# Kernel tuning notes

Hardware: AMD Instinct MI355X
Metric: run time of the kernel (lower is better)

The kernel has to match this reference:

```python
import jax, jax.numpy as jnp
import numpy as np

FA, FB_CAT, FM, HID = 133, 147, 8, 100  # atom feat, bond feat (concat), mol feat, hidden
N_ATOMS, N_BONDS, N_MOLS, MAX_NB = 250000, 500000, 10000, 6
DEPTH = 3


def setup_inputs() -> dict:
    key = jax.random.key(0)
    ks = jax.random.split(key, 10)
    f_atoms = jax.random.normal(ks[0], (N_ATOMS, FA), jnp.float32)
    f_bonds = jax.random.normal(ks[1], (N_BONDS, FB_CAT), jnp.float32)
    f_mol = jax.random.normal(ks[2], (N_MOLS, FM), jnp.float32)
    a2b = jax.random.randint(ks[3], (N_ATOMS, MAX_NB), 0, N_BONDS, jnp.int32)
    b2a = jax.random.randint(ks[4], (N_BONDS,), 0, N_ATOMS, jnp.int32)
    b2revb = jax.random.randint(ks[5], (N_BONDS,), 0, N_BONDS, jnp.int32)
    # contiguous molecules of 25 atoms each -> equivalent of ascope segments
    mol_id = (jnp.arange(N_ATOMS, dtype=jnp.int32) // (N_ATOMS // N_MOLS))
    # parameters (Linear with bias=False): stored as (in, out)
    W_i = jax.random.normal(ks[6], (FB_CAT, HID), jnp.float32) * 0.05
    W_h = jax.random.normal(ks[7], (HID, HID), jnp.float32) * 0.05
    W_o = jax.random.normal(ks[8], (HID + FA, HID), jnp.float32) * 0.05
    return {"f_atoms": f_atoms, "f_bonds": f_bonds, "f_mol": f_mol,
            "W_i": W_i, "W_h": W_h, "W_o": W_o,
            "a2b": a2b, "b2a": b2a, "b2revb": b2revb,
            "mol_id": mol_id, "n_mols": N_MOLS}


def reference(f_atoms, f_bonds, f_mol, W_i, W_h, W_o, a2b, b2a, b2revb, mol_id, n_mols):
    act = jax.nn.relu
    inp = act(f_bonds @ W_i)              # (B, H)
    message = inp
    for _ in range(DEPTH - 1):
        nei = message[a2b]                # (A, MAX_NB, H) gather
        a_message = nei.sum(axis=1)       # (A, H)
        message = a_message[b2a] - message[b2revb]  # (B, H)
        message = act(inp + message @ W_h)
        # dropout p=0 (eval) -> identity
    # readout to atoms
    a_message = message[a2b].sum(axis=1)  # (A, H)
    a_input = jnp.concatenate([f_atoms, a_message], axis=1)  # (A, FA+H)
    atom_hiddens = act(a_input @ W_o)     # (A, H)
    # per-molecule mean over ragged segments (ascope equivalent)
    mol_sum = jax.ops.segment_sum(atom_hiddens, mol_id, num_segments=n_mols)
    counts = jax.ops.segment_sum(jnp.ones((atom_hiddens.shape[0],), atom_hiddens.dtype),
                                 mol_id, num_segments=n_mols)
    mol_vecs = mol_sum / jnp.maximum(counts, 1.0)[:, None]  # zero-vec for empty mols
    mol_vecs = jnp.concatenate([mol_vecs, f_mol], axis=1)   # (M, H+FM)
    return mol_vecs, atom_hiddens
```

## Files before the change

### kernel.cpp

```cpp
#include <hip/hip_runtime.h>

#define THREADS 256

typedef __bf16 bf16x8 __attribute__((ext_vector_type(8)));
typedef float f32x4 __attribute__((ext_vector_type(4)));
typedef float f32x4u __attribute__((ext_vector_type(4), aligned(4)));

__device__ __forceinline__ unsigned short f2b(float x) {
    unsigned int u = __float_as_uint(x);
    u = (u + 0x7FFFu + ((u >> 16) & 1u)) >> 16;
    return (unsigned short)u;
}
__device__ __forceinline__ float b2f(unsigned short h) {
    return __uint_as_float(((unsigned int)h) << 16);
}
__device__ __forceinline__ bf16x8 as_bf(uint4 q) {
    union { uint4 q; bf16x8 v; } u; u.q = q; return u.v;
}

__global__ __launch_bounds__(64) void pack_w(const float* __restrict__ W,
                                             unsigned short* __restrict__ out, int K)
{
    int bid = blockIdx.x;
    int kc = bid / 7, nt = bid - kc * 7;
    int l = threadIdx.x;
    int k0 = kc * 32 + (l >> 4) * 8;
    int n = nt * 16 + (l & 15);
    unsigned short v[8];
    #pragma unroll
    for (int j = 0; j < 8; ++j) {
        int k = k0 + j;
        float x = (k < K && n < 100) ? W[(size_t)k * 100 + n] : 0.f;
        v[j] = f2b(x);
    }
    *(uint4*)&out[((size_t)bid * 64 + l) * 8] = *(uint4*)v;
}

__global__ __launch_bounds__(64) void pack_wo(const float* __restrict__ W,
                                              unsigned short* __restrict__ out)
{
    int bid = blockIdx.x;
    int kc = bid / 7, nt = bid - kc * 7;
    int l = threadIdx.x;
    int k0 = kc * 32 + (l >> 4) * 8;
    int n = nt * 16 + (l & 15);
    unsigned short v[8];
    #pragma unroll
    for (int j = 0; j < 8; ++j) {
        int k = k0 + j;
        float x = 0.f;
        if (n < 100) {
            if (k < 100)                 x = W[(size_t)(133 + k) * 100 + n];
            else if (k >= 112 && k < 245) x = W[(size_t)(k - 112) * 100 + n];
        }
        v[j] = f2b(x);
    }
    *(uint4*)&out[((size_t)bid * 64 + l) * 8] = *(uint4*)v;
}

__global__ __launch_bounds__(THREADS) void gather_sum_bf16(
    const unsigned short* __restrict__ msg, const int* __restrict__ a2b,
    unsigned short* __restrict__ amsg, int A)
{
    int t = blockIdx.x * THREADS + threadIdx.x;
    if (t >= A * 14) return;
    int a = t / 14;
    int c = t - a * 14;
    const int* nb = a2b + (size_t)a * 6;
    float s[8];
    #pragma unroll
    for (int e = 0; e < 8; ++e) s[e] = 0.f;
    #pragma unroll
    for (int j = 0; j < 6; ++j) {
        uint4 v = *(const uint4*)&msg[(size_t)nb[j] * 112 + c * 8];
        const unsigned short* pv = (const unsigned short*)&v;
        #pragma unroll
        for (int e = 0; e < 8; ++e) s[e] += b2f(pv[e]);
    }
    unsigned short r[8];
    #pragma unroll
    for (int e = 0; e < 8; ++e) r[e] = f2b(s[e]);
    *(uint4*)&amsg[(size_t)a * 112 + c * 8] = *(uint4*)r;
}

__global__ __launch_bounds__(THREADS) void gemm_in(
    const float* __restrict__ fb, const unsigned short* __restrict__ wf,
    unsigned short* __restrict__ Y, int M)
{
    __shared__ unsigned short Os[64 * 136];
    const int tid = threadIdx.x;
    const int l = tid & 63, w = tid >> 6;
    const int quad = l >> 4, c15 = l & 15;
    const int row0 = blockIdx.x * 64;
    const int rc = min(row0 + w * 16 + c15, M - 1);
    const float* rowp = fb + (size_t)rc * 147;

    uint4 af[5];
    #pragma unroll
    for (int kc = 0; kc < 4; ++kc) {
        f32x4u x0 = *(const f32x4u*)(rowp + kc * 32 + quad * 8);
        f32x4u x1 = *(const f32x4u*)(rowp + kc * 32 + quad * 8 + 4);
        unsigned short t[8];
        #pragma unroll
        for (int e = 0; e < 4; ++e) { t[e] = f2b(x0[e]); t[4 + e] = f2b(x1[e]); }
        af[kc] = *(uint4*)t;
    }
    {
        unsigned short t[8];
        #pragma unroll
        for (int j = 0; j < 8; ++j) {
            int k = 128 + quad * 8 + j;
            t[j] = (k < 147) ? f2b(rowp[k]) : (unsigned short)0;
        }
        af[4] = *(uint4*)t;
    }

    f32x4 acc[7];
    #pragma unroll
    for (int nt = 0; nt < 7; ++nt) acc[nt] = (f32x4){0.f, 0.f, 0.f, 0.f};
    #pragma unroll
    for (int kc = 0; kc < 5; ++kc) {
        #pragma unroll
        for (int nt = 0; nt < 7; ++nt) {
            uint4 bq = *(const uint4*)&wf[((size_t)(kc * 7 + nt) * 64 + l) * 8];
            acc[nt] = __builtin_amdgcn_mfma_f32_16x16x32_bf16(as_bf(af[kc]), as_bf(bq), acc[nt], 0, 0, 0);
        }
    }

    #pragma unroll
    for (int nt = 0; nt < 7; ++nt)
        #pragma unroll
        for (int reg = 0; reg < 4; ++reg)
            Os[(w * 16 + quad * 4 + reg) * 136 + nt * 16 + c15] = f2b(fmaxf(acc[nt][reg], 0.f));
    __syncthreads();

    for (int t = tid; t < 64 * 14; t += THREADS) {
        int rl = t / 14, c = t - rl * 14;
        int rr = row0 + rl;
        if (rr < M)
            *(uint4*)&Y[(size_t)rr * 112 + c * 8] = *(const uint4*)&Os[rl * 136 + c * 8];
    }
}

__global__ __launch_bounds__(THREADS) void gemm_msg(
    const unsigned short* __restrict__ amsg, const unsigned short* __restrict__ msg,
    const int* __restrict__ b2a, const int* __restrict__ b2revb,
    const unsigned short* __restrict__ wf, const unsigned short* __restrict__ bias,
    unsigned short* __restrict__ Y, int M)
{
    __shared__ unsigned short Os[64 * 136];
    const int tid = threadIdx.x;
    const int l = tid & 63, w = tid >> 6;
    const int quad = l >> 4, c15 = l & 15;
    const int row0 = blockIdx.x * 64;
    const int rc = min(row0 + w * 16 + c15, M - 1);
    const int iA = b2a[rc], iB = b2revb[rc];
    const unsigned short* pa = amsg + (size_t)iA * 112 + quad * 8;
    const unsigned short* pb = msg  + (size_t)iB * 112 + quad * 8;

    uint4 a1[4], a2[4];
    #pragma unroll
    for (int kc = 0; kc < 4; ++kc) {
        a1[kc] = *(const uint4*)(pa + kc * 32);
        a2[kc] = *(const uint4*)(pb + kc * 32);
    }

    f32x4 acc1[7], acc2[7];
    #pragma unroll
    for (int nt = 0; nt < 7; ++nt) {
        acc1[nt] = (f32x4){0.f, 0.f, 0.f, 0.f};
        acc2[nt] = (f32x4){0.f, 0.f, 0.f, 0.f};
    }
    #pragma unroll
    for (int kc = 0; kc < 4; ++kc) {
        #pragma unroll
        for (int nt = 0; nt < 7; ++nt) {
            uint4 bq = *(const uint4*)&wf[((size_t)(kc * 7 + nt) * 64 + l) * 8];
            acc1[nt] = __builtin_amdgcn_mfma_f32_16x16x32_bf16(as_bf(a1[kc]), as_bf(bq), acc1[nt], 0, 0, 0);
            acc2[nt] = __builtin_amdgcn_mfma_f32_16x16x32_bf16(as_bf(a2[kc]), as_bf(bq), acc2[nt], 0, 0, 0);
        }
    }

    #pragma unroll
    for (int nt = 0; nt < 7; ++nt)
        #pragma unroll
        for (int reg = 0; reg < 4; ++reg)
            Os[(w * 16 + quad * 4 + reg) * 136 + nt * 16 + c15] = f2b(acc1[nt][reg] - acc2[nt][reg]);
    __syncthreads();

    for (int t = tid; t < 64 * 14; t += THREADS) {
        int rl = t / 14, c = t - rl * 14;
        int rr = row0 + rl;
        if (rr < M) {
            uint4 o = *(const uint4*)&Os[rl * 136 + c * 8];
            uint4 bq = *(const uint4*)&bias[(size_t)rr * 112 + c * 8];
            const unsigned short* po = (const unsigned short*)&o;
            const unsigned short* pq = (const unsigned short*)&bq;
            unsigned short res[8];
            #pragma unroll
            for (int e = 0; e < 8; ++e)
                res[e] = f2b(fmaxf(b2f(po[e]) + b2f(pq[e]), 0.f));
            *(uint4*)&Y[(size_t)rr * 112 + c * 8] = *(uint4*)res;
        }
    }
}

__global__ __launch_bounds__(THREADS) void gemm_out(
    const float* __restrict__ fa, const unsigned short* __restrict__ amsg,
    const unsigned short* __restrict__ wf, float* __restrict__ Y, int M)
{
    constexpr int KS = 264;
    __shared__ char smem[64 * KS * 2];
    unsigned short* Xs = (unsigned short*)smem;
    float* Os = (float*)smem;

    const int tid = threadIdx.x;
    const int l = tid & 63, w = tid >> 6;
    const int quad = l >> 4, c15 = l & 15;
    const int row0 = blockIdx.x * 64;

    for (int t = tid; t < 64 * 33; t += THREADS) {
        int rl = t / 33, c = t - rl * 33;
        int rr = min(row0 + rl, M - 1);
        uint4 o;
        if (c < 14) {
            o = *(const uint4*)&amsg[(size_t)rr * 112 + c * 8];
        } else if (c < 30) {
            int cc = c - 14;
            f32x4u x0 = *(const f32x4u*)(fa + (size_t)rr * 133 + cc * 8);
            f32x4u x1 = *(const f32x4u*)(fa + (size_t)rr * 133 + cc * 8 + 4);
            unsigned short tt[8];
            #pragma unroll
            for (int e = 0; e < 4; ++e) { tt[e] = f2b(x0[e]); tt[4 + e] = f2b(x1[e]); }
            o = *(uint4*)tt;
        } else if (c == 30) {
            unsigned short tt[8];
            #pragma unroll
            for (int j = 0; j < 8; ++j) {
                int col = 128 + j;
                tt[j] = (col < 133) ? f2b(fa[(size_t)rr * 133 + col]) : (unsigned short)0;
            }
            o = *(uint4*)tt;
        } else {
            o = make_uint4(0u, 0u, 0u, 0u);
        }
        *(uint4*)&Xs[(size_t)rl * KS + c * 8] = o;
    }
    __syncthreads();

    f32x4 acc[7];
    #pragma unroll
    for (int nt = 0; nt < 7; ++nt) acc[nt] = (f32x4){0.f, 0.f, 0.f, 0.f};
    const unsigned short* xrow = Xs + (size_t)(w * 16 + c15) * KS + quad * 8;
    #pragma unroll
    for (int kc = 0; kc < 8; ++kc) {
        bf16x8 av = *(const bf16x8*)(xrow + kc * 32);
        #pragma unroll
        for (int nt = 0; nt < 7; ++nt) {
            uint4 bq = *(const uint4*)&wf[((size_t)(kc * 7 + nt) * 64 + l) * 8];
            acc[nt] = __builtin_amdgcn_mfma_f32_16x16x32_bf16(av, as_bf(bq), acc[nt], 0, 0, 0);
        }
    }
    __syncthreads();

    #pragma unroll
    for (int nt = 0; nt < 7; ++nt) {
        int n = nt * 16 + c15;
        if (n < 100) {
            #pragma unroll
            for (int reg = 0; reg < 4; ++reg)
                Os[(w * 16 + quad * 4 + reg) * 108 + n] = fmaxf(acc[nt][reg], 0.f);
        }
    }
    __syncthreads();

    for (int t = tid; t < 64 * 25; t += THREADS) {
        int rl = t / 25, c = t - rl * 25;
        int rr = row0 + rl;
        if (rr < M)
            *(f32x4*)&Y[(size_t)rr * 100 + c * 4] = *(const f32x4*)&Os[rl * 108 + c * 4];
    }
}

__global__ __launch_bounds__(128) void readout(
    const float* __restrict__ atom_h, const float* __restrict__ f_mol,
    const int* __restrict__ mol_id, int n_atoms, float* __restrict__ out_mol)
{
    int m = blockIdx.x;
    int lo = 0, hi = n_atoms;
    while (lo < hi) { int mid = (lo + hi) >> 1; if (mol_id[mid] < m) lo = mid + 1; else hi = mid; }
    int lo2 = lo, hi2 = n_atoms;
    while (lo2 < hi2) { int mid = (lo2 + hi2) >> 1; if (mol_id[mid] < m + 1) lo2 = mid + 1; else hi2 = mid; }
    float inv = 1.0f / fmaxf((float)(lo2 - lo), 1.0f);
    int c = threadIdx.x;
    if (c < 100) {
        float s = 0.f;
        for (int a = lo; a < lo2; ++a) s += atom_h[(size_t)a * 100 + c];
        out_mol[(size_t)m * 108 + c] = s * inv;
    } else if (c < 108) {
        out_mol[(size_t)m * 108 + c] = f_mol[(size_t)m * 8 + (c - 100)];
    }
}

extern "C" void kernel_launch(void* const* d_in, const int* in_sizes, int n_in,
                              void* d_out, int out_size, void* d_ws, size_t ws_size,
                              hipStream_t stream)
{
    const float* f_atoms = (const float*)d_in[0];
    const float* f_bonds = (const float*)d_in[1];
    const float* f_mol   = (const float*)d_in[2];
    const float* W_i     = (const float*)d_in[3];
    const float* W_h     = (const float*)d_in[4];
    const float* W_o     = (const float*)d_in[5];
    const int* a2b    = (const int*)d_in[6];
    const int* b2a    = (const int*)d_in[7];
    const int* b2revb = (const int*)d_in[8];
    const int* mol_id = (const int*)d_in[9];

    const int A    = in_sizes[0] / 133;
    const int B    = in_sizes[1] / 147;
    const int Mmol = in_sizes[2] / 8;

    unsigned short* wsu = (unsigned short*)d_ws;
    unsigned short* wfi  = wsu;
    unsigned short* wfh  = wfi + 35 * 512;
    unsigned short* wfo  = wfh + 28 * 512;
    unsigned short* amsg = wfo + 56 * 512;
    unsigned short* inp  = amsg + (size_t)A * 112;
    unsigned short* msgA = inp  + (size_t)B * 112;
    unsigned short* msgB = msgA + (size_t)B * 112;

    float* out     = (float*)d_out;
    float* out_mol = out;
    float* atom_h  = out + (size_t)Mmol * 108;

    dim3 blk(THREADS);
    int gB = (B + 63) / 64;
    int gA = (A + 63) / 64;
    int gg = (A * 14 + THREADS - 1) / THREADS;

    pack_w<<<35, dim3(64), 0, stream>>>(W_i, wfi, 147);
    pack_w<<<28, dim3(64), 0, stream>>>(W_h, wfh, 100);
    pack_wo<<<56, dim3(64), 0, stream>>>(W_o, wfo);

    gemm_in<<<gB, blk, 0, stream>>>(f_bonds, wfi, inp, B);

    gather_sum_bf16<<<gg, blk, 0, stream>>>(inp, a2b, amsg, A);
    gemm_msg<<<gB, blk, 0, stream>>>(amsg, inp, b2a, b2revb, wfh, inp, msgA, B);

    gather_sum_bf16<<<gg, blk, 0, stream>>>(msgA, a2b, amsg, A);
    gemm_msg<<<gB, blk, 0, stream>>>(amsg, msgA, b2a, b2revb, wfh, inp, msgB, B);

    gather_sum_bf16<<<gg, blk, 0, stream>>>(msgB, a2b, amsg, A);
    gemm_out<<<gA, blk, 0, stream>>>(f_atoms, amsg, wfo, atom_h, A);

    readout<<<Mmol, dim3(128), 0, stream>>>(atom_h, f_mol, mol_id, A, out_mol);
}
```

Baseline: 1.097 ms.

## Pad message rows to 128 and fuse final neighbor gather into output GEMM

Changes the bf16 message/atom-message row stride from 112 to 128 elements, writing zeros into the pad columns so gathered rows are 256-byte aligned. Also removes the last gather_sum kernel by computing the neighbor sum directly inside gemm_out's tile load. This saves one launch and a round trip of the atom-message buffer through memory, and may make the random gathers more cache-line friendly. In exchange, every message write grows by the pad bytes and the workspace gets larger.

```diff
diff --git a/kernel.cpp b/kernel.cpp
--- a/kernel.cpp
+++ b/kernel.cpp
@@ -1,6 +1,7 @@
 #include <hip/hip_runtime.h>
 
 #define THREADS 256
+#define MS 128
 
 typedef __bf16 bf16x8 __attribute__((ext_vector_type(8)));
 typedef float f32x4 __attribute__((ext_vector_type(4)));
@@ -63,16 +64,20 @@
     unsigned short* __restrict__ amsg, int A)
 {
     int t = blockIdx.x * THREADS + threadIdx.x;
-    if (t >= A * 14) return;
-    int a = t / 14;
-    int c = t - a * 14;
+    if (t >= A * 16) return;
+    int a = t >> 4;
+    int c = t & 15;
+    if (c >= 14) {
+        *(uint4*)&amsg[(size_t)a * MS + c * 8] = make_uint4(0u, 0u, 0u, 0u);
+        return;
+    }
     const int* nb = a2b + (size_t)a * 6;
     float s[8];
     #pragma unroll
     for (int e = 0; e < 8; ++e) s[e] = 0.f;
     #pragma unroll
     for (int j = 0; j < 6; ++j) {
-        uint4 v = *(const uint4*)&msg[(size_t)nb[j] * 112 + c * 8];
+        uint4 v = *(const uint4*)&msg[(size_t)nb[j] * MS + c * 8];
         const unsigned short* pv = (const unsigned short*)&v;
         #pragma unroll
         for (int e = 0; e < 8; ++e) s[e] += b2f(pv[e]);
@@ -80,7 +85,7 @@
     unsigned short r[8];
     #pragma unroll
     for (int e = 0; e < 8; ++e) r[e] = f2b(s[e]);
-    *(uint4*)&amsg[(size_t)a * 112 + c * 8] = *(uint4*)r;
+    *(uint4*)&amsg[(size_t)a * MS + c * 8] = *(uint4*)r;
 }
 
 __global__ __launch_bounds__(THREADS) void gemm_in(
@@ -134,11 +139,14 @@
             Os[(w * 16 + quad * 4 + reg) * 136 + nt * 16 + c15] = f2b(fmaxf(acc[nt][reg], 0.f));
     __syncthreads();
 
-    for (int t = tid; t < 64 * 14; t += THREADS) {
-        int rl = t / 14, c = t - rl * 14;
+    for (int t = tid; t < 64 * 16; t += THREADS) {
+        int rl = t >> 4, c = t & 15;
         int rr = row0 + rl;
-        if (rr < M)
-            *(uint4*)&Y[(size_t)rr * 112 + c * 8] = *(const uint4*)&Os[rl * 136 + c * 8];
+        if (rr < M) {
+            uint4 o = (c < 14) ? *(const uint4*)&Os[rl * 136 + c * 8]
+                               : make_uint4(0u, 0u, 0u, 0u);
+            *(uint4*)&Y[(size_t)rr * MS + c * 8] = o;
+        }
     }
 }
 
@@ -155,8 +163,8 @@
     const int row0 = blockIdx.x * 64;
     const int rc = min(row0 + w * 16 + c15, M - 1);
     const int iA = b2a[rc], iB = b2revb[rc];
-    const unsigned short* pa = amsg + (size_t)iA * 112 + quad * 8;
-    const unsigned short* pb = msg  + (size_t)iB * 112 + quad * 8;
+    const unsigned short* pa = amsg + (size_t)iA * MS + quad * 8;
+    const unsigned short* pb = msg  + (size_t)iB * MS + quad * 8;
 
     uint4 a1[4], a2[4];
     #pragma unroll
@@ -188,25 +196,29 @@
             Os[(w * 16 + quad * 4 + reg) * 136 + nt * 16 + c15] = f2b(acc1[nt][reg] - acc2[nt][reg]);
     __syncthreads();
 
-    for (int t = tid; t < 64 * 14; t += THREADS) {
-        int rl = t / 14, c = t - rl * 14;
+    for (int t = tid; t < 64 * 16; t += THREADS) {
+        int rl = t >> 4, c = t & 15;
         int rr = row0 + rl;
-        if (rr < M) {
+        if (rr >= M) continue;
+        if (c < 14) {
             uint4 o = *(const uint4*)&Os[rl * 136 + c * 8];
-            uint4 bq = *(const uint4*)&bias[(size_t)rr * 112 + c * 8];
+            uint4 bq = *(const uint4*)&bias[(size_t)rr * MS + c * 8];
             const unsigned short* po = (const unsigned short*)&o;
             const unsigned short* pq = (const unsigned short*)&bq;
             unsigned short res[8];
             #pragma unroll
             for (int e = 0; e < 8; ++e)
                 res[e] = f2b(fmaxf(b2f(po[e]) + b2f(pq[e]), 0.f));
-            *(uint4*)&Y[(size_t)rr * 112 + c * 8] = *(uint4*)res;
+            *(uint4*)&Y[(size_t)rr * MS + c * 8] = *(uint4*)res;
+        } else {
+            *(uint4*)&Y[(size_t)rr * MS + c * 8] = make_uint4(0u, 0u, 0u, 0u);
         }
     }
 }
 
 __global__ __launch_bounds__(THREADS) void gemm_out(
-    const float* __restrict__ fa, const unsigned short* __restrict__ amsg,
+    const float* __restrict__ fa, const unsigned short* __restrict__ msg,
+    const int* __restrict__ a2b,
     const unsigned short* __restrict__ wf, float* __restrict__ Y, int M)
 {
     constexpr int KS = 264;
@@ -224,7 +236,21 @@
         int rr = min(row0 + rl, M - 1);
         uint4 o;
         if (c < 14) {
-            o = *(const uint4*)&amsg[(size_t)rr * 112 + c * 8];
+            const int* nb = a2b + (size_t)rr * 6;
+            float s[8];
+            #pragma unroll
+            for (int e = 0; e < 8; ++e) s[e] = 0.f;
+            #pragma unroll
+            for (int j = 0; j < 6; ++j) {
+                uint4 v = *(const uint4*)&msg[(size_t)nb[j] * MS + c * 8];
+                const unsigned short* pv = (const unsigned short*)&v;
+                #pragma unroll
+                for (int e = 0; e < 8; ++e) s[e] += b2f(pv[e]);
+            }
+            unsigned short r[8];
+            #pragma unroll
+            for (int e = 0; e < 8; ++e) r[e] = f2b(s[e]);
+            o = *(uint4*)r;
         } else if (c < 30) {
             int cc = c - 14;
             f32x4u x0 = *(const f32x4u*)(fa + (size_t)rr * 133 + cc * 8);
@@ -326,9 +352,9 @@
     unsigned short* wfh  = wfi + 35 * 512;
     unsigned short* wfo  = wfh + 28 * 512;
     unsigned short* amsg = wfo + 56 * 512;
-    unsigned short* inp  = amsg + (size_t)A * 112;
-    unsigned short* msgA = inp  + (size_t)B * 112;
-    unsigned short* msgB = msgA + (size_t)B * 112;
+    unsigned short* inp  = amsg + (size_t)A * MS;
+    unsigned short* msgA = inp  + (size_t)B * MS;
+    unsigned short* msgB = msgA + (size_t)B * MS;
 
     float* out     = (float*)d_out;
     float* out_mol = out;
@@ -337,7 +363,7 @@
     dim3 blk(THREADS);
     int gB = (B + 63) / 64;
     int gA = (A + 63) / 64;
-    int gg = (A * 14 + THREADS - 1) / THREADS;
+    int gg = (A * 16 + THREADS - 1) / THREADS;
 
     pack_w<<<35, dim3(64), 0, stream>>>(W_i, wfi, 147);
     pack_w<<<28, dim3(64), 0, stream>>>(W_h, wfh, 100);
@@ -351,8 +377,7 @@
     gather_sum_bf16<<<gg, blk, 0, stream>>>(msgA, a2b, amsg, A);
     gemm_msg<<<gB, blk, 0, stream>>>(amsg, msgA, b2a, b2revb, wfh, inp, msgB, B);
 
-    gather_sum_bf16<<<gg, blk, 0, stream>>>(msgB, a2b, amsg, A);
-    gemm_out<<<gA, blk, 0, stream>>>(f_atoms, amsg, wfo, atom_h, A);
+    gemm_out<<<gA, blk, 0, stream>>>(f_atoms, msgB, a2b, wfo, atom_h, A);
 
     readout<<<Mmol, dim3(128), 0, stream>>>(atom_h, f_mol, mol_id, A, out_mol);
 }
```

After: 1.041 ms. 5.1% less time.
